# Kernel optimization log

Measured on AMD Instinct MI355X. Metric: run time of the kernel, lower is better.

## Reference

```python
import jax, jax.numpy as jnp
import numpy as np
from jax import lax

K = 3  # neighbors, as in torch_geometric.nn.knn_interpolate default
EPS = 1e-16


def knn_interpolate(x, pos_x, pos_y):
    """Interpolate features x defined at pos_x onto query points pos_y.
    x: [Ns, F], pos_x: [Ns, 3], pos_y: [Nq, 3] -> [Nq, F].
    Inverse squared-distance weighting over K nearest neighbors."""
    # squared distances via the |y|^2 + |x|^2 - 2 y.x expansion (no [Nq,Ns,3] temp)
    d2 = (jnp.sum(pos_y * pos_y, -1, keepdims=True)
          + jnp.sum(pos_x * pos_x, -1)[None, :]
          - 2.0 * pos_y @ pos_x.T)                      # [Nq, Ns]
    neg_d2, idx = lax.top_k(-d2, K)                      # [Nq, K]
    w = 1.0 / jnp.clip(-neg_d2, EPS)                     # inverse squared distance
    w = w / jnp.sum(w, -1, keepdims=True)
    return jnp.einsum('qk,qkf->qf', w, x[idx])           # gather + weighted reduce


def mlp(x, W1, b1, W2, b2, W3, b3):
    x = jax.nn.relu(x @ W1 + b1)
    x = jax.nn.relu(x @ W2 + b2)
    return x @ W3 + b3


def setup_inputs() -> dict:
    key = jax.random.key(0)
    ks = jax.random.split(key, 16)
    Nh, Nl, H, O = 16384, 4096, 256, 3
    s = lambda fan: 1.0 / np.sqrt(fan)
    return {
        'emb1':  jax.random.normal(ks[0], (Nh, H), jnp.float32),
        'l_y1':  jax.random.normal(ks[1], (Nl, O), jnp.float32),
        'l_pos1': jax.random.uniform(ks[2], (Nl, 3), jnp.float32),
        'h_pos1': jax.random.uniform(ks[3], (Nh, 3), jnp.float32),
        'emb2':  jax.random.normal(ks[4], (Nh, H), jnp.float32),
        'l_y2':  jax.random.normal(ks[5], (Nl, O), jnp.float32),
        'l_pos2': jax.random.uniform(ks[6], (Nl, 3), jnp.float32),
        'h_pos2': jax.random.uniform(ks[7], (Nh, 3), jnp.float32),
        'W1': jax.random.uniform(ks[8], (H, H), jnp.float32, -s(H), s(H)),
        'b1': jax.random.uniform(ks[9], (H,), jnp.float32, -s(H), s(H)),
        'W2': jax.random.uniform(ks[10], (H, H), jnp.float32, -s(H), s(H)),
        'b2': jax.random.uniform(ks[11], (H,), jnp.float32, -s(H), s(H)),
        'W3': jax.random.uniform(ks[12], (H, O), jnp.float32, -s(H), s(H)),
        'b3': jax.random.uniform(ks[13], (O,), jnp.float32, -s(H), s(H)),
    }


def reference(emb1, l_y1, l_pos1, h_pos1, emb2, l_y2, l_pos2, h_pos2,
              W1, b1, W2, b2, W3, b3):
    x = mlp(emb1 - knn_interpolate(emb2, h_pos2, h_pos1), W1, b1, W2, b2, W3, b3)
    # residual=True branch
    res = knn_interpolate(l_y1 - knn_interpolate(l_y2, l_pos2, l_pos1), l_pos1, h_pos1)
    return x + res
```

## Files before the change

### kernel.cpp

```cpp
#include <hip/hip_runtime.h>
#include <math.h>

#define BIGF 3.0e38f

typedef short  s16x8 __attribute__((ext_vector_type(8)));
typedef float  f32x4 __attribute__((ext_vector_type(4)));

__device__ __forceinline__ unsigned short f2bf(float x) {
  unsigned int b = __float_as_uint(x);
  unsigned int r = b + 0x7FFFu + ((b >> 16) & 1u);
  return (unsigned short)(r >> 16);
}
__device__ __forceinline__ float bf2f(unsigned short h) {
  return __uint_as_float(((unsigned int)h) << 16);
}


__device__ __forceinline__ int cell_clamp(float v, int G) {
  int c = (int)(v * (float)G);
  return min(G - 1, max(0, c));
}

__device__ __forceinline__ void ins3(float d, int id,
                                     float& d0, float& d1, float& d2,
                                     int& i0, int& i1, int& i2) {
  bool l0 = (d < d0) || (d == d0 && id < i0);
  bool l1 = (d < d1) || (d == d1 && id < i1);
  bool l2 = (d < d2) || (d == d2 && id < i2);
  float nd0 = l0 ? d  : d0;  int ni0 = l0 ? id : i0;
  float nd1 = l0 ? d0 : (l1 ? d  : d1);
  int   ni1 = l0 ? i0 : (l1 ? id : i1);
  float nd2 = l1 ? d1 : (l2 ? d  : d2);
  int   ni2 = l1 ? i1 : (l2 ? id : i2);
  d0 = nd0; d1 = nd1; d2 = nd2; i0 = ni0; i1 = ni1; i2 = ni2;
}

__device__ __forceinline__ void scan_shell(
    int R, int sl, int G, int cx, int cy, int cz,
    const int* __restrict__ offs, const float4* __restrict__ spts,
    const int* __restrict__ sidx,
    float qx, float qy, float qz, float sy,
    float& d0, float& d1, float& d2v, int& i0, int& i1, int& i2)
{
  #pragma clang fp contract(off)
  #define SCANP()                                                             \
    { int j = js;                                                             \
      if (j < je) {                                                           \
        float4 sc = spts[j]; int idc = sidx[j];                               \
        for (++j; ; ++j) {                                                    \
          bool more = (j < je);                                               \
          float4 sn; int idn;                                                 \
          if (more) { sn = spts[j]; idn = sidx[j]; }                          \
          float p0 = qx * sc.x, p1 = qy * sc.y, p2 = qz * sc.z;               \
          float dt = (p0 + p1) + p2;                                          \
          float S  = sy + sc.w;                                               \
          float dd = S - 2.0f * dt;                                           \
          ins3(dd, idc, d0, d1, d2v, i0, i1, i2);                             \
          if (!more) break;                                                   \
          sc = sn; idc = idn;                                                 \
        }                                                                     \
      } }

  if (R == 1) {
    if (sl < 9) {
      int dy = sl % 3 - 1, dz = sl / 3 - 1;
      int yy = cy + dy, zz = cz + dz;
      if (yy >= 0 && yy < G && zz >= 0 && zz < G) {
        int xs = max(cx - 1, 0), xe = min(cx + 1, G - 1);
        int base = (zz * G + yy) * G;
        int js = offs[base + xs], je = offs[base + xe + 1];
        SCANP()
      }
    }
  } else {
    const int twoR1 = 2 * R + 1, inner = 2 * R - 1;
    const int nfz = 2 * twoR1;
    const int nfull = nfz + 2 * inner;
    const int half = inner * inner;
    const int nitems = nfull + 2 * half;
    for (int m = sl; m < nitems; m += 16) {
      int dy, dz, js, je;
      if (m < nfull) {
        if (m < nfz) { dz = (m < twoR1) ? -R : R; dy = (m % twoR1) - R; }
        else { int u = m - nfz; dy = (u < inner) ? -R : R; dz = (u % inner) - (R - 1); }
        int yy = cy + dy, zz = cz + dz;
        if (yy < 0 || yy >= G || zz < 0 || zz >= G) continue;
        int xs = max(cx - R, 0), xe = min(cx + R, G - 1);
        int base = (zz * G + yy) * G;
        js = offs[base + xs]; je = offs[base + xe + 1];
      } else {
        int u = m - nfull;
        int xc = (u < half) ? (cx - R) : (cx + R);
        int r2 = (u < half) ? u : u - half;
        dy = r2 % inner - (R - 1); dz = r2 / inner - (R - 1);
        int yy = cy + dy, zz = cz + dz;
        if (xc < 0 || xc >= G || yy < 0 || yy >= G || zz < 0 || zz >= G) continue;
        int c = (zz * G + yy) * G + xc;
        js = offs[c]; je = offs[c + 1];
      }
      SCANP()
    }
  }
  #undef SCANP
}

#define MERGE16(E0, E1, E2, J0, J1, J2)                                       \
  { _Pragma("unroll")                                                         \
    for (int msk = 1; msk < 16; msk <<= 1) {                                  \
      float o0 = __shfl_xor(E0, msk), o1 = __shfl_xor(E1, msk), o2 = __shfl_xor(E2, msk); \
      int   p0 = __shfl_xor(J0, msk), p1 = __shfl_xor(J1, msk), p2 = __shfl_xor(J2, msk); \
      ins3(o0, p0, E0, E1, E2, J0, J1, J2);                                   \
      ins3(o1, p1, E0, E1, E2, J0, J1, J2);                                   \
      ins3(o2, p2, E0, E1, E2, J0, J1, J2);                                   \
    } }

__device__ void knn_dualgrid_body(
    int bid,
    const float4* __restrict__ qspts, const int* __restrict__ qsidx, int Nq,
    int GA, const int* __restrict__ offsA, const float4* __restrict__ sptsA, const int* __restrict__ sidxA,
    float* __restrict__ wA_out, int* __restrict__ iA_out,
    int GB, const int* __restrict__ offsB, const float4* __restrict__ sptsB, const int* __restrict__ sidxB,
    float* __restrict__ wB_out, int* __restrict__ iB_out)
{
  #pragma clang fp contract(off)
  const int sl = threadIdx.x & 15;
  const int qs = bid * 16 + (threadIdx.x >> 4);
  if (qs >= Nq) return;

  float4 qv = qspts[qs];
  const float qx = qv.x, qy = qv.y, qz = qv.z;
  const float sy = qv.w;
  const int qorig = qsidx[qs];
  const float csA = 1.0f / (float)GA, csB = 1.0f / (float)GB;
  const int cxA = cell_clamp(qx, GA), cyA = cell_clamp(qy, GA), czA = cell_clamp(qz, GA);
  const int cxB = cell_clamp(qx, GB), cyB = cell_clamp(qy, GB), czB = cell_clamp(qz, GB);

  float a0 = BIGF, a1 = BIGF, a2 = BIGF;  int ia0 = -1, ia1 = -1, ia2 = -1;
  float b0 = BIGF, b1 = BIGF, b2 = BIGF;  int ib0 = -1, ib1 = -1, ib2 = -1;
  float eA0 = BIGF, eA1 = BIGF, eA2 = BIGF; int jA0 = -1, jA1 = -1, jA2 = -1;
  float eB0 = BIGF, eB1 = BIGF, eB2 = BIGF; int jB0 = -1, jB1 = -1, jB2 = -1;
  bool doneA = false, doneB = false;

  const int Gmax = max(GA, GB);
  for (int R = 1; R <= Gmax; ++R) {
    if (!doneA && R <= GA)
      scan_shell(R, sl, GA, cxA, cyA, czA, offsA, sptsA, sidxA,
                 qx, qy, qz, sy, a0, a1, a2, ia0, ia1, ia2);
    if (!doneB && R <= GB)
      scan_shell(R, sl, GB, cxB, cyB, czB, offsB, sptsB, sidxB,
                 qx, qy, qz, sy, b0, b1, b2, ib0, ib1, ib2);
    if (!doneA && R <= GA) {
      eA0 = a0; eA1 = a1; eA2 = a2; jA0 = ia0; jA1 = ia1; jA2 = ia2;
      MERGE16(eA0, eA1, eA2, jA0, jA1, jA2)
      float bnd = (float)R * csA;
      doneA = (eA2 <= bnd * bnd - 1e-6f) || (R >= GA);
    }
    if (!doneB && R <= GB) {
      eB0 = b0; eB1 = b1; eB2 = b2; jB0 = ib0; jB1 = ib1; jB2 = ib2;
      MERGE16(eB0, eB1, eB2, jB0, jB1, jB2)
      float bnd = (float)R * csB;
      doneB = (eB2 <= bnd * bnd - 1e-6f) || (R >= GB);
    }
    if (__all(doneA && doneB)) break;
  }

  if (sl == 0) {
    {
      float w0 = 1.0f / fmaxf(eA0, 1e-16f);
      float w1 = 1.0f / fmaxf(eA1, 1e-16f);
      float w2 = 1.0f / fmaxf(eA2, 1e-16f);
      float inv = 1.0f / (w0 + w1 + w2);
      wA_out[(size_t)qorig * 3 + 0] = w0 * inv;
      wA_out[(size_t)qorig * 3 + 1] = w1 * inv;
      wA_out[(size_t)qorig * 3 + 2] = w2 * inv;
      iA_out[(size_t)qorig * 3 + 0] = jA0;
      iA_out[(size_t)qorig * 3 + 1] = jA1;
      iA_out[(size_t)qorig * 3 + 2] = jA2;
    }
    {
      float w0 = 1.0f / fmaxf(eB0, 1e-16f);
      float w1 = 1.0f / fmaxf(eB1, 1e-16f);
      float w2 = 1.0f / fmaxf(eB2, 1e-16f);
      float inv = 1.0f / (w0 + w1 + w2);
      wB_out[(size_t)qorig * 3 + 0] = w0 * inv;
      wB_out[(size_t)qorig * 3 + 1] = w1 * inv;
      wB_out[(size_t)qorig * 3 + 2] = w2 * inv;
      iB_out[(size_t)qorig * 3 + 0] = jB0;
      iB_out[(size_t)qorig * 3 + 1] = jB1;
      iB_out[(size_t)qorig * 3 + 2] = jB2;
    }
  }
}

__device__ void knn_single_body(
    int bid,
    const float4* __restrict__ qspts, const int* __restrict__ qsidx, int Nq, int G,
    const int* __restrict__ offs, const float4* __restrict__ spts, const int* __restrict__ sidx,
    const float* __restrict__ base3, const float* __restrict__ feat3,
    float* __restrict__ out3)
{
  #pragma clang fp contract(off)
  const int sl = threadIdx.x & 15;
  const int qs = bid * 16 + (threadIdx.x >> 4);
  if (qs >= Nq) return;

  float4 qv = qspts[qs];
  const float qx = qv.x, qy = qv.y, qz = qv.z;
  const float sy = qv.w;
  const int qorig = qsidx[qs];
  const float cs = 1.0f / (float)G;
  const int cx = cell_clamp(qx, G), cy = cell_clamp(qy, G), cz = cell_clamp(qz, G);

  float d0 = BIGF, d1 = BIGF, d2v = BIGF;
  int i0 = -1, i1 = -1, i2 = -1;
  float e0 = BIGF, e1 = BIGF, e2 = BIGF;
  int j0 = -1, j1 = -1, j2 = -1;
  bool done = false;

  for (int R = 1; R <= G; ++R) {
    if (!done) {
      scan_shell(R, sl, G, cx, cy, cz, offs, spts, sidx,
                 qx, qy, qz, sy, d0, d1, d2v, i0, i1, i2);
      e0 = d0; e1 = d1; e2 = d2v; j0 = i0; j1 = i1; j2 = i2;
      MERGE16(e0, e1, e2, j0, j1, j2)
      float bnd = (float)R * cs;
      done = (e2 <= bnd * bnd - 1e-6f) || (R >= G);
    }
    if (__all(done)) break;
  }

  if (sl == 0) {
    float w0 = 1.0f / fmaxf(e0, 1e-16f);
    float w1 = 1.0f / fmaxf(e1, 1e-16f);
    float w2 = 1.0f / fmaxf(e2, 1e-16f);
    float inv = 1.0f / (w0 + w1 + w2);
    w0 *= inv; w1 *= inv; w2 *= inv;
    #pragma unroll
    for (int f = 0; f < 3; ++f) {
      float v = w0 * feat3[(size_t)j0 * 3 + f]
              + w1 * feat3[(size_t)j1 * 3 + f]
              + w2 * feat3[(size_t)j2 * 3 + f];
      out3[(size_t)qorig * 3 + f] = base3[(size_t)qorig * 3 + f] - v;
    }
  }
}

__device__ void build_t_body(
    int bid, const float* __restrict__ emb1, const float* __restrict__ emb2,
    const float* __restrict__ w, const int* __restrict__ idx,
    unsigned short* __restrict__ t_hi, unsigned short* __restrict__ t_lo, int Nq)
{
  int gid = bid * 256 + threadIdx.x;
  int q = gid >> 6, c4 = gid & 63;
  if (q >= Nq) return;
  float w0 = w[(size_t)q * 3 + 0], w1 = w[(size_t)q * 3 + 1], w2 = w[(size_t)q * 3 + 2];
  int i0 = idx[(size_t)q * 3 + 0], i1 = idx[(size_t)q * 3 + 1], i2 = idx[(size_t)q * 3 + 2];
  const float4* e1 = (const float4*)emb1;
  const float4* e2 = (const float4*)emb2;
  float4 a  = e1[(size_t)q * 64 + c4];
  float4 f0 = e2[(size_t)i0 * 64 + c4];
  float4 f1 = e2[(size_t)i1 * 64 + c4];
  float4 f2 = e2[(size_t)i2 * 64 + c4];
  float4 r;
  r.x = a.x - (w0 * f0.x + w1 * f1.x + w2 * f2.x);
  r.y = a.y - (w0 * f0.y + w1 * f1.y + w2 * f2.y);
  r.z = a.z - (w0 * f0.z + w1 * f1.z + w2 * f2.z);
  r.w = a.w - (w0 * f0.w + w1 * f1.w + w2 * f2.w);
  ushort4 h, l;
  h.x = f2bf(r.x); l.x = f2bf(r.x - bf2f(h.x));
  h.y = f2bf(r.y); l.y = f2bf(r.y - bf2f(h.y));
  h.z = f2bf(r.z); l.z = f2bf(r.z - bf2f(h.z));
  h.w = f2bf(r.w); l.w = f2bf(r.w - bf2f(h.w));
  size_t o = (size_t)q * 256 + c4 * 4;
  *(ushort4*)&t_hi[o] = h;
  *(ushort4*)&t_lo[o] = l;
}

__device__ void res_gather_body(
    int bid, const float* __restrict__ wC, const int* __restrict__ idxC,
    const float* __restrict__ diff, float* __restrict__ res, int Nq)
{
  int q = bid * 256 + threadIdx.x;
  if (q >= Nq) return;
  float w0 = wC[(size_t)q * 3 + 0], w1 = wC[(size_t)q * 3 + 1], w2 = wC[(size_t)q * 3 + 2];
  int i0 = idxC[(size_t)q * 3 + 0], i1 = idxC[(size_t)q * 3 + 1], i2 = idxC[(size_t)q * 3 + 2];
  #pragma unroll
  for (int f = 0; f < 3; ++f) {
    res[(size_t)q * 3 + f] = w0 * diff[(size_t)i0 * 3 + f]
                           + w1 * diff[(size_t)i1 * 3 + f]
                           + w2 * diff[(size_t)i2 * 3 + f];
  }
}

__global__ __launch_bounds__(256) void knn_fused_kernel(
    const float4* qspts, const int* qsidx, int Nh,
    int G1, const int* offs1, const float4* spts1, const int* sidx1, float* wA, int* idxA,
    int G2, const int* offs3, const float4* spts3, const int* sidx3, float* wC, int* idxC,
    int Nl, const int* offs2, const float4* spts2, const int* sidx2,
    const float* l_y1, const float* l_y2, float* diff)
{
  int g = blockIdx.x / 5, r = blockIdx.x % 5;
  if (r < 4)
    knn_dualgrid_body(g * 4 + r, qspts, qsidx, Nh,
                      G1, offs1, spts1, sidx1, wA, idxA,
                      G2, offs3, spts3, sidx3, wC, idxC);
  else
    knn_single_body(g, spts3, sidx3, Nl, G2, offs2, spts2, sidx2,
                    l_y1, l_y2, diff);
}

__global__ __launch_bounds__(256) void bt_gather_kernel(
    const float* emb1, const float* emb2, const float* w, const int* idx,
    unsigned short* t_hi, unsigned short* t_lo, int Nq_bt,
    const float* wC, const int* idxC, const float* diff, float* res, int NqG)
{
  if (blockIdx.x < 64)
    res_gather_body(blockIdx.x, wC, idxC, diff, res, NqG);
  else
    build_t_body(blockIdx.x - 64, emb1, emb2, w, idx, t_hi, t_lo, Nq_bt);
}

__global__ __launch_bounds__(256) void zero_kernel(int* __restrict__ p, int n) {
  int i = blockIdx.x * 256 + threadIdx.x;
  if (i < n) p[i] = 0;
}

__global__ __launch_bounds__(256) void count_split_kernel(
    const float* __restrict__ p1, int n1, int g1, int* __restrict__ c1,
    const float* __restrict__ p2, int n2, int g2, int* __restrict__ c2,
    const float* __restrict__ p3, int n3, int g3, int* __restrict__ c3,
    const float* __restrict__ p4, int n4, int g4, int* __restrict__ c4,
    const float* __restrict__ W1, unsigned short* __restrict__ h1T, unsigned short* __restrict__ l1T,
    const float* __restrict__ W2, unsigned short* __restrict__ h2T, unsigned short* __restrict__ l2T)
{
  int b = blockIdx.x;
  if (b >= 160) {
    int sb = b - 160;
    const float* W = (sb < 256) ? W1 : W2;
    unsigned short* hiT = (sb < 256) ? h1T : h2T;
    unsigned short* loT = (sb < 256) ? l1T : l2T;
    int id = (sb & 255) * 256 + threadIdx.x;
    int k = id >> 8, n = id & 255;
    float x = W[id];
    unsigned short h = f2bf(x);
    unsigned short l = f2bf(x - bf2f(h));
    hiT[n * 256 + k] = h;
    loT[n * 256 + k] = l;
    return;
  }
  const float* p; int n, G; int* cnt; int i;
  if (b < 64)       { p = p1; n = n1; G = g1; cnt = c1; i = b * 256 + threadIdx.x; }
  else if (b < 80)  { p = p2; n = n2; G = g2; cnt = c2; i = (b - 64) * 256 + threadIdx.x; }
  else if (b < 96)  { p = p3; n = n3; G = g3; cnt = c3; i = (b - 80) * 256 + threadIdx.x; }
  else              { p = p4; n = n4; G = g4; cnt = c4; i = (b - 96) * 256 + threadIdx.x; }
  if (i >= n) return;
  int cx = cell_clamp(p[3 * i],     G);
  int cy = cell_clamp(p[3 * i + 1], G);
  int cz = cell_clamp(p[3 * i + 2], G);
  atomicAdd(&cnt[(cz * G + cy) * G + cx], 1);
}

__global__ __launch_bounds__(256) void prefix4_kernel(
    const int* __restrict__ c1, int* __restrict__ o1, int* __restrict__ u1, int m1,
    const int* __restrict__ c2, int* __restrict__ o2, int* __restrict__ u2, int m2,
    const int* __restrict__ c3, int* __restrict__ o3, int* __restrict__ u3, int m3,
    const int* __restrict__ c4, int* __restrict__ o4, int* __restrict__ u4, int m4)
{
  const int* cnt; int* offs; int* cur; int M;
  if (blockIdx.x == 0)      { cnt = c1; offs = o1; cur = u1; M = m1; }
  else if (blockIdx.x == 1) { cnt = c2; offs = o2; cur = u2; M = m2; }
  else if (blockIdx.x == 2) { cnt = c3; offs = o3; cur = u3; M = m3; }
  else                      { cnt = c4; offs = o4; cur = u4; M = m4; }
  __shared__ int ps[256];
  const int tid = threadIdx.x;
  const int per = (M + 255) >> 8;
  const int base = tid * per;
  int s = 0;
  for (int j = 0; j < per; ++j) if (base + j < M) s += cnt[base + j];
  ps[tid] = s;
  __syncthreads();
  for (int off = 1; off < 256; off <<= 1) {
    int v = (tid >= off) ? ps[tid - off] : 0;
    __syncthreads();
    ps[tid] += v;
    __syncthreads();
  }
  int run = (tid > 0) ? ps[tid - 1] : 0;
  for (int j = 0; j < per; ++j) {
    if (base + j < M) {
      offs[base + j] = run; cur[base + j] = run;
      run += cnt[base + j];
    }
  }
  if (tid == 255) offs[M] = run;
}

__global__ __launch_bounds__(256) void scatter4_kernel(
    const float* __restrict__ p1, int n1, int g1, int* __restrict__ u1, float4* __restrict__ s1, int* __restrict__ x1,
    const float* __restrict__ p2, int n2, int g2, int* __restrict__ u2, float4* __restrict__ s2, int* __restrict__ x2,
    const float* __restrict__ p3, int n3, int g3, int* __restrict__ u3, float4* __restrict__ s3, int* __restrict__ x3,
    const float* __restrict__ p4, int n4, int g4, int* __restrict__ u4, float4* __restrict__ s4, int* __restrict__ x4)
{
  #pragma clang fp contract(off)
  int b = blockIdx.x;
  const float* p; int n, G; int* cur; float4* spts; int* sidx; int i;
  if (b < 64)       { p = p1; n = n1; G = g1; cur = u1; spts = s1; sidx = x1; i = b * 256 + threadIdx.x; }
  else if (b < 80)  { p = p2; n = n2; G = g2; cur = u2; spts = s2; sidx = x2; i = (b - 64) * 256 + threadIdx.x; }
  else if (b < 96)  { p = p3; n = n3; G = g3; cur = u3; spts = s3; sidx = x3; i = (b - 80) * 256 + threadIdx.x; }
  else              { p = p4; n = n4; G = g4; cur = u4; spts = s4; sidx = x4; i = (b - 96) * 256 + threadIdx.x; }
  if (i >= n) return;
  float x = p[3 * i], y = p[3 * i + 1], z = p[3 * i + 2];
  int cx = cell_clamp(x, G), cy = cell_clamp(y, G), cz = cell_clamp(z, G);
  int c = (cz * G + cy) * G + cx;
  int pos = atomicAdd(&cur[c], 1);
  float sx = (x * x + y * y) + z * z;
  spts[pos] = make_float4(x, y, z, sx);
  sidx[pos] = i;
}

__global__ __launch_bounds__(256) void mfma_gemm_kernel(
    const unsigned short* __restrict__ A_hi, const unsigned short* __restrict__ A_lo,
    const unsigned short* __restrict__ BT_hi, const unsigned short* __restrict__ BT_lo,
    const float* __restrict__ bias,
    float* __restrict__ outf,
    unsigned short* __restrict__ out_hi, unsigned short* __restrict__ out_lo,
    int relu, int split_out)
{
  __shared__ unsigned short Bs_hi[64][132];
  __shared__ unsigned short Bs_lo[64][132];
  const int t = threadIdx.x;
  const int d = blockIdx.x;
  const int xcd = d & 7, slot = d >> 3;
  const int lin = xcd * ((int)gridDim.x >> 3) + slot;
  const int row0 = (lin >> 2) * 64;
  const int col0 = (lin & 3) * 64;

  const int l = t & 63, w = t >> 6;
  const int lr = l & 15;
  const int lk = (l >> 4) << 3;
  const unsigned short* arh = A_hi + (size_t)(row0 + w * 16 + lr) * 256;
  const unsigned short* arl = A_lo + (size_t)(row0 + w * 16 + lr) * 256;

  const int sc = t >> 2;
  const int sk = (t & 3) << 5;

  f32x4 acc0 = {0.f,0.f,0.f,0.f}, acc1 = {0.f,0.f,0.f,0.f};
  f32x4 acc2 = {0.f,0.f,0.f,0.f}, acc3 = {0.f,0.f,0.f,0.f};

  #define KSTEP(CT, ACC)                                                      \
    { s16x8 bh = *(const s16x8*)&Bs_hi[CT * 16 + lr][kc + lk];                \
      s16x8 bl = *(const s16x8*)&Bs_lo[CT * 16 + lr][kc + lk];                \
      ACC = __builtin_amdgcn_mfma_f32_16x16x32_bf16(ah, bh, ACC, 0, 0, 0);    \
      ACC = __builtin_amdgcn_mfma_f32_16x16x32_bf16(al, bh, ACC, 0, 0, 0);    \
      ACC = __builtin_amdgcn_mfma_f32_16x16x32_bf16(ah, bl, ACC, 0, 0, 0); }

  for (int half = 0; half < 2; ++half) {
    if (half) __syncthreads();
    {
      const int4* sh = (const int4*)&BT_hi[(size_t)(col0 + sc) * 256 + half * 128 + sk];
      const int4* slo = (const int4*)&BT_lo[(size_t)(col0 + sc) * 256 + half * 128 + sk];
      int4* dh = (int4*)&Bs_hi[sc][sk];
      int4* dl = (int4*)&Bs_lo[sc][sk];
      #pragma unroll
      for (int i = 0; i < 4; ++i) { dh[i] = sh[i]; dl[i] = slo[i]; }
    }
    __syncthreads();
    const int kbase = half * 128;
    #pragma unroll
    for (int kc = 0; kc < 128; kc += 32) {
      s16x8 ah = *(const s16x8*)&arh[kbase + kc + lk];
      s16x8 al = *(const s16x8*)&arl[kbase + kc + lk];
      KSTEP(0, acc0)
      KSTEP(1, acc1)
      KSTEP(2, acc2)
      KSTEP(3, acc3)
    }
  }
  #undef KSTEP

  const int orow = row0 + w * 16 + ((l >> 4) << 2);
  #define EPILOG(CT, ACC)                                                     \
    { int col = col0 + CT * 16 + lr;                                          \
      float bb = bias[col];                                                   \
      _Pragma("unroll")                                                       \
      for (int r = 0; r < 4; ++r) {                                           \
        float v = ACC[r] + bb;                                                \
        if (relu) v = fmaxf(v, 0.0f);                                         \
        size_t o = (size_t)(orow + r) * 256 + col;                            \
        if (split_out) {                                                      \
          unsigned short hh = f2bf(v);                                        \
          out_hi[o] = hh; out_lo[o] = f2bf(v - bf2f(hh));                     \
        } else {                                                              \
          outf[o] = v;                                                        \
        }                                                                     \
      } }
  EPILOG(0, acc0)
  EPILOG(1, acc1)
  EPILOG(2, acc2)
  EPILOG(3, acc3)
  #undef EPILOG
}

__global__ __launch_bounds__(256) void final_kernel(
    const float* __restrict__ h2, const float* __restrict__ W3,
    const float* __restrict__ b3, const float* __restrict__ res,
    float* __restrict__ out, int M)
{
  __shared__ float sW3[768];
  const int tid = threadIdx.x;
  for (int i = tid; i < 768; i += 256) sW3[i] = W3[i];
  __syncthreads();

  const int wave = tid >> 6, lane = tid & 63;
  const int r = blockIdx.x * 4 + wave;
  if (r >= M) return;

  float4 h = ((const float4*)h2)[(size_t)r * 64 + lane];
  const int c = lane * 4;
  float a0 = h.x * sW3[(c + 0) * 3 + 0] + h.y * sW3[(c + 1) * 3 + 0]
           + h.z * sW3[(c + 2) * 3 + 0] + h.w * sW3[(c + 3) * 3 + 0];
  float a1 = h.x * sW3[(c + 0) * 3 + 1] + h.y * sW3[(c + 1) * 3 + 1]
           + h.z * sW3[(c + 2) * 3 + 1] + h.w * sW3[(c + 3) * 3 + 1];
  float a2 = h.x * sW3[(c + 0) * 3 + 2] + h.y * sW3[(c + 1) * 3 + 2]
           + h.z * sW3[(c + 2) * 3 + 2] + h.w * sW3[(c + 3) * 3 + 2];

  #pragma unroll
  for (int off = 32; off; off >>= 1) {
    a0 += __shfl_xor(a0, off);
    a1 += __shfl_xor(a1, off);
    a2 += __shfl_xor(a2, off);
  }
  if (lane == 0) {
    out[(size_t)r * 3 + 0] = a0 + b3[0] + res[(size_t)r * 3 + 0];
    out[(size_t)r * 3 + 1] = a1 + b3[1] + res[(size_t)r * 3 + 1];
    out[(size_t)r * 3 + 2] = a2 + b3[2] + res[(size_t)r * 3 + 2];
  }
}

extern "C" void kernel_launch(void* const* d_in, const int* in_sizes, int n_in,
                              void* d_out, int out_size, void* d_ws, size_t ws_size,
                              hipStream_t stream) {
  (void)in_sizes; (void)n_in; (void)out_size; (void)ws_size;
  const float* emb1   = (const float*)d_in[0];
  const float* l_y1   = (const float*)d_in[1];
  const float* l_pos1 = (const float*)d_in[2];
  const float* h_pos1 = (const float*)d_in[3];
  const float* emb2   = (const float*)d_in[4];
  const float* l_y2   = (const float*)d_in[5];
  const float* l_pos2 = (const float*)d_in[6];
  const float* h_pos2 = (const float*)d_in[7];
  const float* W1     = (const float*)d_in[8];
  const float* b1     = (const float*)d_in[9];
  const float* W2     = (const float*)d_in[10];
  const float* b2     = (const float*)d_in[11];
  const float* W3     = (const float*)d_in[12];
  const float* b3     = (const float*)d_in[13];
  float* out = (float*)d_out;

  const int Nh = 16384, Nl = 4096, H = 256;
  const int G1 = 16, G2 = 10;
  const int M1 = G1 * G1 * G1, M2 = G2 * G2 * G2;

  char* wsp = (char*)d_ws;
  size_t off = 0;
  auto alloc = [&](size_t bytes) -> void* {
    void* p = wsp + off;
    off += (bytes + 255) & ~(size_t)255;
    return p;
  };
  int*            idxA   = (int*)           alloc((size_t)Nh * 3 * 4);
  float*          wA     = (float*)         alloc((size_t)Nh * 3 * 4);
  int*            idxC   = (int*)           alloc((size_t)Nh * 3 * 4);
  float*          wC     = (float*)         alloc((size_t)Nh * 3 * 4);
  unsigned short* t_hi   = (unsigned short*)alloc((size_t)Nh * H * 2);
  unsigned short* t_lo   = (unsigned short*)alloc((size_t)Nh * H * 2);
  unsigned short* h1_hi  = (unsigned short*)alloc((size_t)Nh * H * 2);
  unsigned short* h1_lo  = (unsigned short*)alloc((size_t)Nh * H * 2);
  float*          h2     = (float*)t_hi;
  unsigned short* w1t_hi = (unsigned short*)alloc((size_t)H * H * 2);
  unsigned short* w1t_lo = (unsigned short*)alloc((size_t)H * H * 2);
  unsigned short* w2t_hi = (unsigned short*)alloc((size_t)H * H * 2);
  unsigned short* w2t_lo = (unsigned short*)alloc((size_t)H * H * 2);
  float*          diff   = (float*)         alloc((size_t)Nl * 3 * 4);
  float*          res    = (float*)         alloc((size_t)Nh * 3 * 4);
  int*            cnts   = (int*)           alloc((size_t)(M1 + M2 + M2 + M1) * 4);
  int* cnt1 = cnts, *cnt2 = cnts + M1, *cnt3 = cnts + M1 + M2, *cnt4 = cnts + M1 + 2 * M2;
  int*            offs1  = (int*)           alloc((size_t)(M1 + 1) * 4);
  int*            cur1   = (int*)           alloc((size_t)M1 * 4);
  int*            offs2  = (int*)           alloc((size_t)(M2 + 1) * 4);
  int*            cur2   = (int*)           alloc((size_t)M2 * 4);
  int*            offs3  = (int*)           alloc((size_t)(M2 + 1) * 4);
  int*            cur3   = (int*)           alloc((size_t)M2 * 4);
  int*            offs4  = (int*)           alloc((size_t)(M1 + 1) * 4);
  int*            cur4   = (int*)           alloc((size_t)M1 * 4);
  float4*         spts1  = (float4*)        alloc((size_t)Nh * 16);
  int*            sidx1  = (int*)           alloc((size_t)Nh * 4);
  float4*         spts2  = (float4*)        alloc((size_t)Nl * 16);
  int*            sidx2  = (int*)           alloc((size_t)Nl * 4);
  float4*         spts3  = (float4*)        alloc((size_t)Nl * 16);
  int*            sidx3  = (int*)           alloc((size_t)Nl * 4);
  float4*         qspts  = (float4*)        alloc((size_t)Nh * 16);
  int*            qsidx  = (int*)           alloc((size_t)Nh * 4);

  const int ncnt = M1 + M2 + M2 + M1;
  zero_kernel<<<(ncnt + 255) / 256, 256, 0, stream>>>(cnts, ncnt);
  count_split_kernel<<<672, 256, 0, stream>>>(
      h_pos2, Nh, G1, cnt1,  l_pos2, Nl, G2, cnt2,
      l_pos1, Nl, G2, cnt3,  h_pos1, Nh, G1, cnt4,
      W1, w1t_hi, w1t_lo, W2, w2t_hi, w2t_lo);
  prefix4_kernel<<<4, 256, 0, stream>>>(
      cnt1, offs1, cur1, M1,  cnt2, offs2, cur2, M2,
      cnt3, offs3, cur3, M2,  cnt4, offs4, cur4, M1);
  scatter4_kernel<<<160, 256, 0, stream>>>(
      h_pos2, Nh, G1, cur1, spts1, sidx1,
      l_pos2, Nl, G2, cur2, spts2, sidx2,
      l_pos1, Nl, G2, cur3, spts3, sidx3,
      h_pos1, Nh, G1, cur4, qspts, qsidx);

  knn_fused_kernel<<<1280, 256, 0, stream>>>(
      qspts, qsidx, Nh,
      G1, offs1, spts1, sidx1, wA, idxA,
      G2, offs3, spts3, sidx3, wC, idxC,
      Nl, offs2, spts2, sidx2, l_y1, l_y2, diff);

  bt_gather_kernel<<<4160, 256, 0, stream>>>(
      emb1, emb2, wA, idxA, t_hi, t_lo, Nh,
      wC, idxC, diff, res, Nh);

  mfma_gemm_kernel<<<(Nh / 64) * 4, 256, 0, stream>>>(
      t_hi, t_lo, w1t_hi, w1t_lo, b1, nullptr, h1_hi, h1_lo, 1, 1);
  mfma_gemm_kernel<<<(Nh / 64) * 4, 256, 0, stream>>>(
      h1_hi, h1_lo, w2t_hi, w2t_lo, b2, h2, nullptr, nullptr, 1, 0);

  final_kernel<<<Nh / 4, 256, 0, stream>>>(h2, W3, b3, res, out, Nh);
}
```

Measured before the change: 127.8 us.

## Fuse embedding gather into KNN kernel and residual gather into first GEMM

New measurement: 119.5 us. 1.07x faster.

```diff
diff --git a/kernel.cpp b/kernel.cpp
--- a/kernel.cpp
+++ b/kernel.cpp
@@ -114,15 +114,15 @@
       ins3(o2, p2, E0, E1, E2, J0, J1, J2);                                   \
     } }
 
-__device__ void knn_dualgrid_body(
+__device__ void knn_bt_body(
     int bid,
     const float4* __restrict__ qspts, const int* __restrict__ qsidx, int Nq,
     int GA, const int* __restrict__ offsA, const float4* __restrict__ sptsA, const int* __restrict__ sidxA,
-    float* __restrict__ wA_out, int* __restrict__ iA_out,
     int GB, const int* __restrict__ offsB, const float4* __restrict__ sptsB, const int* __restrict__ sidxB,
-    float* __restrict__ wB_out, int* __restrict__ iB_out)
-{
-  #pragma clang fp contract(off)
+    float* __restrict__ wC_out, int* __restrict__ iC_out,
+    const float* __restrict__ emb1, const float* __restrict__ emb2,
+    unsigned short* __restrict__ t_hi, unsigned short* __restrict__ t_lo)
+{
   const int sl = threadIdx.x & 15;
   const int qs = bid * 16 + (threadIdx.x >> 4);
   if (qs >= Nq) return;
@@ -165,29 +165,46 @@
   }
 
   if (sl == 0) {
-    {
-      float w0 = 1.0f / fmaxf(eA0, 1e-16f);
-      float w1 = 1.0f / fmaxf(eA1, 1e-16f);
-      float w2 = 1.0f / fmaxf(eA2, 1e-16f);
-      float inv = 1.0f / (w0 + w1 + w2);
-      wA_out[(size_t)qorig * 3 + 0] = w0 * inv;
-      wA_out[(size_t)qorig * 3 + 1] = w1 * inv;
-      wA_out[(size_t)qorig * 3 + 2] = w2 * inv;
-      iA_out[(size_t)qorig * 3 + 0] = jA0;
-      iA_out[(size_t)qorig * 3 + 1] = jA1;
-      iA_out[(size_t)qorig * 3 + 2] = jA2;
-    }
-    {
-      float w0 = 1.0f / fmaxf(eB0, 1e-16f);
-      float w1 = 1.0f / fmaxf(eB1, 1e-16f);
-      float w2 = 1.0f / fmaxf(eB2, 1e-16f);
-      float inv = 1.0f / (w0 + w1 + w2);
-      wB_out[(size_t)qorig * 3 + 0] = w0 * inv;
-      wB_out[(size_t)qorig * 3 + 1] = w1 * inv;
-      wB_out[(size_t)qorig * 3 + 2] = w2 * inv;
-      iB_out[(size_t)qorig * 3 + 0] = jB0;
-      iB_out[(size_t)qorig * 3 + 1] = jB1;
-      iB_out[(size_t)qorig * 3 + 2] = jB2;
+    float w0 = 1.0f / fmaxf(eB0, 1e-16f);
+    float w1 = 1.0f / fmaxf(eB1, 1e-16f);
+    float w2 = 1.0f / fmaxf(eB2, 1e-16f);
+    float inv = 1.0f / (w0 + w1 + w2);
+    wC_out[(size_t)qorig * 3 + 0] = w0 * inv;
+    wC_out[(size_t)qorig * 3 + 1] = w1 * inv;
+    wC_out[(size_t)qorig * 3 + 2] = w2 * inv;
+    iC_out[(size_t)qorig * 3 + 0] = jB0;
+    iC_out[(size_t)qorig * 3 + 1] = jB1;
+    iC_out[(size_t)qorig * 3 + 2] = jB2;
+  }
+
+  {
+    float w0 = 1.0f / fmaxf(eA0, 1e-16f);
+    float w1 = 1.0f / fmaxf(eA1, 1e-16f);
+    float w2 = 1.0f / fmaxf(eA2, 1e-16f);
+    float inv = 1.0f / (w0 + w1 + w2);
+    w0 *= inv; w1 *= inv; w2 *= inv;
+    const float4* e1 = (const float4*)emb1;
+    const float4* e2 = (const float4*)emb2;
+    #pragma unroll
+    for (int k = 0; k < 4; ++k) {
+      int c4 = sl + 16 * k;
+      float4 a  = e1[(size_t)qorig * 64 + c4];
+      float4 f0 = e2[(size_t)jA0 * 64 + c4];
+      float4 f1 = e2[(size_t)jA1 * 64 + c4];
+      float4 f2 = e2[(size_t)jA2 * 64 + c4];
+      float4 r;
+      r.x = a.x - (w0 * f0.x + w1 * f1.x + w2 * f2.x);
+      r.y = a.y - (w0 * f0.y + w1 * f1.y + w2 * f2.y);
+      r.z = a.z - (w0 * f0.z + w1 * f1.z + w2 * f2.z);
+      r.w = a.w - (w0 * f0.w + w1 * f1.w + w2 * f2.w);
+      ushort4 h, l;
+      h.x = f2bf(r.x); l.x = f2bf(r.x - bf2f(h.x));
+      h.y = f2bf(r.y); l.y = f2bf(r.y - bf2f(h.y));
+      h.z = f2bf(r.z); l.z = f2bf(r.z - bf2f(h.z));
+      h.w = f2bf(r.w); l.w = f2bf(r.w - bf2f(h.w));
+      size_t o = (size_t)qorig * 256 + (size_t)c4 * 4;
+      *(ushort4*)&t_hi[o] = h;
+      *(ushort4*)&t_lo[o] = l;
     }
   }
 }
@@ -245,37 +262,6 @@
   }
 }
 
-__device__ void build_t_body(
-    int bid, const float* __restrict__ emb1, const float* __restrict__ emb2,
-    const float* __restrict__ w, const int* __restrict__ idx,
-    unsigned short* __restrict__ t_hi, unsigned short* __restrict__ t_lo, int Nq)
-{
-  int gid = bid * 256 + threadIdx.x;
-  int q = gid >> 6, c4 = gid & 63;
-  if (q >= Nq) return;
-  float w0 = w[(size_t)q * 3 + 0], w1 = w[(size_t)q * 3 + 1], w2 = w[(size_t)q * 3 + 2];
-  int i0 = idx[(size_t)q * 3 + 0], i1 = idx[(size_t)q * 3 + 1], i2 = idx[(size_t)q * 3 + 2];
-  const float4* e1 = (const float4*)emb1;
-  const float4* e2 = (const float4*)emb2;
-  float4 a  = e1[(size_t)q * 64 + c4];
-  float4 f0 = e2[(size_t)i0 * 64 + c4];
-  float4 f1 = e2[(size_t)i1 * 64 + c4];
-  float4 f2 = e2[(size_t)i2 * 64 + c4];
-  float4 r;
-  r.x = a.x - (w0 * f0.x + w1 * f1.x + w2 * f2.x);
-  r.y = a.y - (w0 * f0.y + w1 * f1.y + w2 * f2.y);
-  r.z = a.z - (w0 * f0.z + w1 * f1.z + w2 * f2.z);
-  r.w = a.w - (w0 * f0.w + w1 * f1.w + w2 * f2.w);
-  ushort4 h, l;
-  h.x = f2bf(r.x); l.x = f2bf(r.x - bf2f(h.x));
-  h.y = f2bf(r.y); l.y = f2bf(r.y - bf2f(h.y));
-  h.z = f2bf(r.z); l.z = f2bf(r.z - bf2f(h.z));
-  h.w = f2bf(r.w); l.w = f2bf(r.w - bf2f(h.w));
-  size_t o = (size_t)q * 256 + c4 * 4;
-  *(ushort4*)&t_hi[o] = h;
-  *(ushort4*)&t_lo[o] = l;
-}
-
 __device__ void res_gather_body(
     int bid, const float* __restrict__ wC, const int* __restrict__ idxC,
     const float* __restrict__ diff, float* __restrict__ res, int Nq)
@@ -292,32 +278,25 @@
   }
 }
 
-__global__ __launch_bounds__(256) void knn_fused_kernel(
+__global__ __launch_bounds__(256) void knn_bt_kernel(
     const float4* qspts, const int* qsidx, int Nh,
-    int G1, const int* offs1, const float4* spts1, const int* sidx1, float* wA, int* idxA,
-    int G2, const int* offs3, const float4* spts3, const int* sidx3, float* wC, int* idxC,
+    int G1, const int* offs1, const float4* spts1, const int* sidx1,
+    int G2, const int* offs3, const float4* spts3, const int* sidx3,
+    float* wC, int* idxC,
+    const float* emb1, const float* emb2,
+    unsigned short* t_hi, unsigned short* t_lo,
     int Nl, const int* offs2, const float4* spts2, const int* sidx2,
     const float* l_y1, const float* l_y2, float* diff)
 {
   int g = blockIdx.x / 5, r = blockIdx.x % 5;
   if (r < 4)
-    knn_dualgrid_body(g * 4 + r, qspts, qsidx, Nh,
-                      G1, offs1, spts1, sidx1, wA, idxA,
-                      G2, offs3, spts3, sidx3, wC, idxC);
+    knn_bt_body(g * 4 + r, qspts, qsidx, Nh,
+                G1, offs1, spts1, sidx1,
+                G2, offs3, spts3, sidx3, wC, idxC,
+                emb1, emb2, t_hi, t_lo);
   else
     knn_single_body(g, spts3, sidx3, Nl, G2, offs2, spts2, sidx2,
                     l_y1, l_y2, diff);
-}
-
-__global__ __launch_bounds__(256) void bt_gather_kernel(
-    const float* emb1, const float* emb2, const float* w, const int* idx,
-    unsigned short* t_hi, unsigned short* t_lo, int Nq_bt,
-    const float* wC, const int* idxC, const float* diff, float* res, int NqG)
-{
-  if (blockIdx.x < 64)
-    res_gather_body(blockIdx.x, wC, idxC, diff, res, NqG);
-  else
-    build_t_body(blockIdx.x - 64, emb1, emb2, w, idx, t_hi, t_lo, Nq_bt);
 }
 
 __global__ __launch_bounds__(256) void zero_kernel(int* __restrict__ p, int n) {
@@ -424,14 +403,20 @@
     const float* __restrict__ bias,
     float* __restrict__ outf,
     unsigned short* __restrict__ out_hi, unsigned short* __restrict__ out_lo,
-    int relu, int split_out)
+    int relu, int split_out, int ngemm,
+    const float* __restrict__ wC, const int* __restrict__ idxC,
+    const float* __restrict__ diff, float* __restrict__ resout, int NqG)
 {
   __shared__ unsigned short Bs_hi[64][132];
   __shared__ unsigned short Bs_lo[64][132];
   const int t = threadIdx.x;
   const int d = blockIdx.x;
+  if (d >= ngemm) {
+    res_gather_body(d - ngemm, wC, idxC, diff, resout, NqG);
+    return;
+  }
   const int xcd = d & 7, slot = d >> 3;
-  const int lin = xcd * ((int)gridDim.x >> 3) + slot;
+  const int lin = xcd * (ngemm >> 3) + slot;
   const int row0 = (lin >> 2) * 64;
   const int col0 = (lin & 3) * 64;
 
@@ -568,8 +553,6 @@
     off += (bytes + 255) & ~(size_t)255;
     return p;
   };
-  int*            idxA   = (int*)           alloc((size_t)Nh * 3 * 4);
-  float*          wA     = (float*)         alloc((size_t)Nh * 3 * 4);
   int*            idxC   = (int*)           alloc((size_t)Nh * 3 * 4);
   float*          wC     = (float*)         alloc((size_t)Nh * 3 * 4);
   unsigned short* t_hi   = (unsigned short*)alloc((size_t)Nh * H * 2);
@@ -617,20 +600,19 @@
       l_pos1, Nl, G2, cur3, spts3, sidx3,
       h_pos1, Nh, G1, cur4, qspts, qsidx);
 
-  knn_fused_kernel<<<1280, 256, 0, stream>>>(
+  knn_bt_kernel<<<1280, 256, 0, stream>>>(
       qspts, qsidx, Nh,
-      G1, offs1, spts1, sidx1, wA, idxA,
+      G1, offs1, spts1, sidx1,
       G2, offs3, spts3, sidx3, wC, idxC,
+      emb1, emb2, t_hi, t_lo,
       Nl, offs2, spts2, sidx2, l_y1, l_y2, diff);
 
-  bt_gather_kernel<<<4160, 256, 0, stream>>>(
-      emb1, emb2, wA, idxA, t_hi, t_lo, Nh,
+  mfma_gemm_kernel<<<1024 + 64, 256, 0, stream>>>(
+      t_hi, t_lo, w1t_hi, w1t_lo, b1, nullptr, h1_hi, h1_lo, 1, 1, 1024,
       wC, idxC, diff, res, Nh);
-
-  mfma_gemm_kernel<<<(Nh / 64) * 4, 256, 0, stream>>>(
-      t_hi, t_lo, w1t_hi, w1t_lo, b1, nullptr, h1_hi, h1_lo, 1, 1);
-  mfma_gemm_kernel<<<(Nh / 64) * 4, 256, 0, stream>>>(
-      h1_hi, h1_lo, w2t_hi, w2t_lo, b2, h2, nullptr, nullptr, 1, 0);
+  mfma_gemm_kernel<<<1024, 256, 0, stream>>>(
+      h1_hi, h1_lo, w2t_hi, w2t_lo, b2, h2, nullptr, nullptr, 1, 0, 1024,
+      nullptr, nullptr, nullptr, nullptr, 0);
 
   final_kernel<<<Nh / 4, 256, 0, stream>>>(h2, W3, b3, res, out, Nh);
 }
```
